# Performance work log

Hardware: AMD Instinct MI355X
Metric: run time of the kernel (lower is better)

The kernel has to match this reference:

```python
import jax, jax.numpy as jnp
import numpy as np


def setup_inputs() -> dict:
    key = jax.random.key(0)
    ks = jax.random.split(key, 9)
    B, T, C, H = 4, 2048, 1024, 16
    hd = C // H  # 64
    s = 0.02
    return {
        "x": jax.random.normal(ks[0], (B, T, C), dtype=jnp.float32),
        "Wq": jax.random.normal(ks[1], (H, C, hd), dtype=jnp.float32) * s,
        "bq": jax.random.normal(ks[2], (H, hd), dtype=jnp.float32) * s,
        "Wk": jax.random.normal(ks[3], (H, C, hd), dtype=jnp.float32) * s,
        "bk": jax.random.normal(ks[4], (H, hd), dtype=jnp.float32) * s,
        "Wv": jax.random.normal(ks[5], (H, C, hd), dtype=jnp.float32) * s,
        "bv": jax.random.normal(ks[6], (H, hd), dtype=jnp.float32) * s,
        "Wp": jax.random.normal(ks[7], (C, C), dtype=jnp.float32) * s,
        "bp": jax.random.normal(ks[8], (C,), dtype=jnp.float32) * s,
    }


def reference(x, Wq, bq, Wk, bk, Wv, bv, Wp, bp):
    B, T, C = x.shape
    # per-head projections, batched over heads: [B,H,T,hd]
    q = jnp.einsum('btc,hcd->bhtd', x, Wq) + bq[None, :, None, :]
    k = jnp.einsum('btc,hcd->bhtd', x, Wk) + bk[None, :, None, :]
    v = jnp.einsum('btc,hcd->bhtd', x, Wv) + bv[None, :, None, :]
    # NOTE: original scales by full embed dim C (not head_size) -- faithful quirk
    scale = jnp.asarray(C, x.dtype) ** -0.5
    wei = jnp.einsum('bhtd,bhsd->bhts', q, k) * scale  # [B,H,T,T]
    causal = jnp.tril(jnp.ones((T, T), dtype=bool))
    wei = jnp.where(causal, wei, jnp.asarray(-jnp.inf, wei.dtype))
    wei = jax.nn.softmax(wei, axis=-1)
    out = jnp.einsum('bhts,bhsd->bhtd', wei, v)  # [B,H,T,hd]
    # concat heads along feature dim -> [B,T,C]
    out = out.transpose(0, 2, 1, 3).reshape(B, T, C)
    return out @ Wp + bp
```

## Files before the change

kernel.cpp:

```cpp
#include <hip/hip_runtime.h>
#include <hip/hip_bf16.h>
#include <stdint.h>


typedef unsigned short u16;
typedef __attribute__((ext_vector_type(4))) float f32x4;
typedef __attribute__((ext_vector_type(8))) __bf16 bf16x8;
typedef __attribute__((ext_vector_type(2))) __bf16 bf16x2;

#define DEV static __device__ __forceinline__

DEV u16 f2bf(float f) {
  uint32_t u = __builtin_bit_cast(uint32_t, f);
  return (u16)((u + 0x7FFFu + ((u >> 16) & 1u)) >> 16);
}

DEV uint pack2(float a, float b) {
  bf16x2 v;
  v.x = (__bf16)a;
  v.y = (__bf16)b;
  return __builtin_bit_cast(uint, v);
}

#if __has_builtin(__builtin_amdgcn_exp2f)
DEV float fexp2(float x) { return __builtin_amdgcn_exp2f(x); }
#else
DEV float fexp2(float x) { return __expf(x * 0.69314718056f); }
#endif

DEV void gload_lds16(const void* g, void* lds) {
  auto gp = reinterpret_cast<const __attribute__((address_space(1))) uint32_t*>(
      reinterpret_cast<uintptr_t>(g));
  auto lp = reinterpret_cast<__attribute__((address_space(3))) uint32_t*>(
      static_cast<uint32_t>(reinterpret_cast<uintptr_t>(lds)));
  __builtin_amdgcn_global_load_lds(gp, lp, 16, 0, 0);
}

DEV f32x4 mfma16(bf16x8 a, bf16x8 b, f32x4 c) {
  return __builtin_amdgcn_mfma_f32_16x16x32_bf16(a, b, c, 0, 0, 0);
}

DEV void bar() {
  asm volatile("" ::: "memory");
  __builtin_amdgcn_s_barrier();
  asm volatile("" ::: "memory");
}

#define LD8(p) (*reinterpret_cast<const bf16x8*>(p))
#define LDU4(p) (*reinterpret_cast<const uint4*>(p))


__global__ void cvt_x_kernel(const float* __restrict__ x, u16* __restrict__ xb, int n8) {
  int i = blockIdx.x * blockDim.x + threadIdx.x;
  int stride = gridDim.x * blockDim.x;
  for (; i < n8; i += stride) {
    const float4* xp = reinterpret_cast<const float4*>(x) + 2 * (size_t)i;
    float4 a = xp[0], b = xp[1];
    uint4 o;
    o.x = pack2(a.x, a.y);
    o.y = pack2(a.z, a.w);
    o.z = pack2(b.x, b.y);
    o.w = pack2(b.z, b.w);
    reinterpret_cast<uint4*>(xb)[i] = o;
  }
}

__global__ void cvt_wqkv_kernel(const float* __restrict__ Wq, const float* __restrict__ Wk,
                                const float* __restrict__ Wv, const float* __restrict__ bq,
                                const float* __restrict__ bk, const float* __restrict__ bv,
                                u16* __restrict__ wt, float* __restrict__ biasq) {
  __shared__ u16 tle[64 * 72];
  const int tid = threadIdx.x;
  const int ct = blockIdx.x;
  const int h = blockIdx.y;
  const int which = blockIdx.z;
  const float* W = (which == 0) ? Wq : (which == 1) ? Wk : Wv;
  const float* Bb = (which == 0) ? bq : (which == 1) ? bk : bv;
  const float scl = (which == 0) ? 0.045084220027780106f : 1.0f;
#pragma unroll
  for (int i = 0; i < 4; ++i) {
    int idx = i * 256 + tid;
    int c_l = idx >> 4, d4 = (idx & 15) * 4;
    float4 v = *reinterpret_cast<const float4*>(&W[((size_t)(h * 1024 + ct * 64 + c_l)) * 64 + d4]);
    tle[(d4 + 0) * 72 + c_l] = f2bf(v.x * scl);
    tle[(d4 + 1) * 72 + c_l] = f2bf(v.y * scl);
    tle[(d4 + 2) * 72 + c_l] = f2bf(v.z * scl);
    tle[(d4 + 3) * 72 + c_l] = f2bf(v.w * scl);
  }
  __syncthreads();
#pragma unroll
  for (int i = 0; i < 2; ++i) {
    int idx = i * 256 + tid;
    int d_o = idx >> 3, c8 = (idx & 7) * 8;
    uint4 v = LDU4(&tle[d_o * 72 + c8]);
    *reinterpret_cast<uint4*>(&wt[(size_t)(which * 1024 + h * 64 + d_o) * 1024 + ct * 64 + c8]) = v;
  }
  if (ct == 0 && tid < 64) biasq[which * 1024 + h * 64 + tid] = Bb[h * 64 + tid] * scl;
}

__global__ void cvt_wp_kernel(const float* __restrict__ Wp, u16* __restrict__ wpt) {
  __shared__ u16 tle[64 * 72];
  const int tid = threadIdx.x;
  const int ct = blockIdx.x;
  const int nt = blockIdx.y;
#pragma unroll
  for (int i = 0; i < 4; ++i) {
    int idx = i * 256 + tid;
    int c_l = idx >> 4, n4 = (idx & 15) * 4;
    float4 v = *reinterpret_cast<const float4*>(&Wp[(size_t)(ct * 64 + c_l) * 1024 + nt * 64 + n4]);
    tle[(n4 + 0) * 72 + c_l] = f2bf(v.x);
    tle[(n4 + 1) * 72 + c_l] = f2bf(v.y);
    tle[(n4 + 2) * 72 + c_l] = f2bf(v.z);
    tle[(n4 + 3) * 72 + c_l] = f2bf(v.w);
  }
  __syncthreads();
#pragma unroll
  for (int i = 0; i < 2; ++i) {
    int idx = i * 256 + tid;
    int n_o = idx >> 3, c8 = (idx & 7) * 8;
    uint4 v = LDU4(&tle[n_o * 72 + c8]);
    *reinterpret_cast<uint4*>(&wpt[(size_t)(nt * 64 + n_o) * 1024 + ct * 64 + c8]) = v;
  }
}

__global__ __launch_bounds__(256)
void transpose_v_kernel(const u16* __restrict__ qkv, u16* __restrict__ vT) {
  __shared__ alignas(16) u16 tle[64 * 72];
  const int tid = threadIdx.x;
  const int tt = blockIdx.x;
  const int h = blockIdx.y;
  const int bb = blockIdx.z;
  const size_t rbase = ((size_t)bb * 2048 + tt * 64) * 3072 + 2048 + h * 64;
#pragma unroll
  for (int i = 0; i < 2; ++i) {
    int idx = i * 256 + tid;
    int s = idx >> 3, c8 = (idx & 7) * 8;
    *reinterpret_cast<uint4*>(&tle[s * 72 + c8]) = LDU4(&qkv[rbase + (size_t)s * 3072 + c8]);
  }
  __syncthreads();
#pragma unroll
  for (int i = 0; i < 2; ++i) {
    int idx = i * 256 + tid;
    int d = idx >> 3, cb = idx & 7;
    uint4 o;
    o.x = (uint)tle[(2 * cb + 0) * 72 + d] | ((uint)tle[(16 + 2 * cb + 0) * 72 + d] << 16);
    o.y = (uint)tle[(32 + 2 * cb + 0) * 72 + d] | ((uint)tle[(48 + 2 * cb + 0) * 72 + d] << 16);
    o.z = (uint)tle[(2 * cb + 1) * 72 + d] | ((uint)tle[(16 + 2 * cb + 1) * 72 + d] << 16);
    o.w = (uint)tle[(32 + 2 * cb + 1) * 72 + d] | ((uint)tle[(48 + 2 * cb + 1) * 72 + d] << 16);
    *reinterpret_cast<uint4*>(
        &vT[((size_t)(bb * 16 + h) * 64 + d) * 2048 + tt * 64 + cb * 8]) = o;
  }
}


template <bool OUT_F32>
__global__ __launch_bounds__(512, 2)
void gemm9_kernel(const u16* __restrict__ A, const u16* __restrict__ Bt,
                  const float* __restrict__ bias, void* __restrict__ Cout,
                  int M, int N, int K, int nbn) {
  __shared__ alignas(16) u16 LA[2 * 8192];
  __shared__ alignas(16) u16 LB[3 * 16384];

  const int tid = threadIdx.x;
  const int lane = tid & 63;
  const int wave = tid >> 6;
  const int wm = wave >> 2;
  const int wn = wave & 3;
  const int fr = lane & 15;
  const int kg = lane >> 4;
  const int f7 = fr & 7;
  const int r4 = kg * 4;

  const int nwg = gridDim.x;
  const int swz = (blockIdx.x & 7) * (nwg >> 3) + (blockIdx.x >> 3);
  const int m0 = (swz / nbn) * 128;
  const int n0 = (swz % nbn) * 256;

  const int NT = K >> 6;

  const int srow = tid >> 3;
  const int sgcol = ((tid & 7) ^ (srow & 7)) << 3;
  const size_t aOff = (size_t)(m0 + srow) * K + sgcol;
  const size_t bOff = (size_t)(n0 + srow) * K + sgcol;
  const int ldst = tid * 8;

  auto stageA = [&](int kt, u16* labuf) {
    gload_lds16(A + aOff + (size_t)kt * 64, labuf + ldst);
    gload_lds16(A + aOff + (size_t)64 * K + (size_t)kt * 64, labuf + 4096 + ldst);
  };
  auto stageB = [&](int kt, u16* lbbuf) {
    gload_lds16(Bt + bOff + (size_t)kt * 64, lbbuf + ldst);
    gload_lds16(Bt + bOff + (size_t)64 * K + (size_t)kt * 64, lbbuf + 4096 + ldst);
    gload_lds16(Bt + bOff + (size_t)128 * K + (size_t)kt * 64, lbbuf + 8192 + ldst);
    gload_lds16(Bt + bOff + (size_t)192 * K + (size_t)kt * 64, lbbuf + 12288 + ldst);
  };

  f32x4 acc[4][4] = {};

  stageA(0, LA);
  stageB(0, LB);
  if (NT > 1) {
    stageB(1, LB + 16384);
    asm volatile("s_waitcnt vmcnt(4)" ::: "memory");
  } else {
    asm volatile("s_waitcnt vmcnt(0)" ::: "memory");
  }
  bar();

  for (int kt = 0; kt < NT; ++kt) {
    const bool st1 = (kt + 1 < NT);
    const bool st2 = (kt + 2 < NT);
    u16* laCur = LA + (kt & 1) * 8192;
    u16* lbCur = LB + (kt % 3) * 16384;

    if (st1) stageA(kt + 1, LA + ((kt + 1) & 1) * 8192);
    if (st2) stageB(kt + 2, LB + ((kt + 2) % 3) * 16384);

    bf16x8 aF[4][2], bF[4][2];
#pragma unroll
    for (int m = 0; m < 4; ++m)
#pragma unroll
      for (int ks = 0; ks < 2; ++ks)
        aF[m][ks] = LD8(&laCur[wm * 4096 + (m * 16 + fr) * 64 + (((ks * 4 + kg) ^ f7) << 3)]);
#pragma unroll
    for (int n = 0; n < 4; ++n)
#pragma unroll
      for (int ks = 0; ks < 2; ++ks)
        bF[n][ks] = LD8(&lbCur[wn * 4096 + (n * 16 + fr) * 64 + (((ks * 4 + kg) ^ f7) << 3)]);

    __builtin_amdgcn_s_setprio(1);
#pragma unroll
    for (int ks = 0; ks < 2; ++ks)
#pragma unroll
      for (int m = 0; m < 4; ++m)
#pragma unroll
        for (int n = 0; n < 4; ++n)
          acc[m][n] = mfma16(aF[m][ks], bF[n][ks], acc[m][n]);
    __builtin_amdgcn_s_setprio(0);

    if (st1) {
      if (st2) asm volatile("s_waitcnt vmcnt(4)" ::: "memory");
      else     asm volatile("s_waitcnt vmcnt(0)" ::: "memory");
      bar();
    }
  }

#pragma unroll
  for (int m = 0; m < 4; ++m) {
    const int row = m0 + wm * 64 + m * 16 + r4;
#pragma unroll
    for (int n = 0; n < 4; ++n) {
      const int col = n0 + wn * 64 + n * 16 + fr;
      const float bv = bias[col];
#pragma unroll
      for (int r = 0; r < 4; ++r) {
        float v = acc[m][n][r] + bv;
        size_t off = (size_t)(row + r) * N + col;
        if constexpr (OUT_F32) reinterpret_cast<float*>(Cout)[off] = v;
        else                   reinterpret_cast<u16*>(Cout)[off] = f2bf(v);
      }
    }
  }
}


__global__ __launch_bounds__(128, 2)
void attn_kernel(const u16* __restrict__ qkv, const u16* __restrict__ vT,
                 u16* __restrict__ obuf) {
  __shared__ alignas(16) u16 Ks[64 * 72];
  __shared__ alignas(16) u16 Vs[64 * 72];
  __shared__ alignas(16) u16 Ps[2][32 * 72];

  const int tid = threadIdx.x;
  const int lane = tid & 63;
  const int wave = tid >> 6;

  const int gid = blockIdx.x;
  const int xcd = gid & 7;
  const int jj = gid >> 3;
  const int g = xcd * 8 + (jj >> 4);
  const int pair = jj & 15;
  const int bb = g >> 4;
  const int h = g & 15;

  const size_t baseQ = (size_t)bb * 2048 * 3072 + h * 64;
  const size_t baseK = baseQ + 1024;
  const size_t baseVt = (size_t)(bb * 16 + h) * 64 * 2048;

  const int fr = lane & 15;
  const int kg8 = (lane >> 4) * 8;
  const int qw32 = wave * 32;
  const int r4 = (lane >> 4) * 4;

  const int rrA = tid >> 3;
  const int cA8 = (tid & 7) * 8;
  const size_t gK = (size_t)rrA * 3072 + cA8;
  const size_t gV = (size_t)rrA * 2048 + cA8;
  const int lof = rrA * 72 + cA8;
  u16* __restrict__ Pw = &Ps[wave][0];

  for (int half = 0; half < 2; ++half) {
    const int qt = half ? (31 - pair) : pair;
    const int q0 = qt * 64;
    const int nt = qt + 1;

    const u16* qrow0 = &qkv[baseQ + (size_t)(q0 + qw32 + fr) * 3072 + kg8];
    bf16x8 aq00 = LD8(qrow0), aq01 = LD8(qrow0 + 32);
    const u16* qrow1 = qrow0 + 16 * 3072;
    bf16x8 aq10 = LD8(qrow1), aq11 = LD8(qrow1 + 32);

    float lsA0 = 0.f, lsA1 = 0.f, lsA2 = 0.f, lsA3 = 0.f;
    float lsB0 = 0.f, lsB1 = 0.f, lsB2 = 0.f, lsB3 = 0.f;
    f32x4 oA0 = {}, oA1 = {}, oA2 = {}, oA3 = {};
    f32x4 oB0 = {}, oB1 = {}, oB2 = {}, oB3 = {};

    uint4 kr0 = LDU4(&qkv[baseK + gK]);
    uint4 kr1 = LDU4(&qkv[baseK + gK + 49152]);
    uint4 kr2 = LDU4(&qkv[baseK + gK + 98304]);
    uint4 kr3 = LDU4(&qkv[baseK + gK + 147456]);
    uint4 vr0 = LDU4(&vT[baseVt + gV]);
    uint4 vr1 = LDU4(&vT[baseVt + gV + 32768]);
    uint4 vr2 = LDU4(&vT[baseVt + gV + 65536]);
    uint4 vr3 = LDU4(&vT[baseVt + gV + 98304]);

    for (int t = 0; t < nt; ++t) {
      __syncthreads();
      *reinterpret_cast<uint4*>(&Ks[lof]) = kr0;
      *reinterpret_cast<uint4*>(&Ks[lof + 1152]) = kr1;
      *reinterpret_cast<uint4*>(&Ks[lof + 2304]) = kr2;
      *reinterpret_cast<uint4*>(&Ks[lof + 3456]) = kr3;
      *reinterpret_cast<uint4*>(&Vs[lof]) = vr0;
      *reinterpret_cast<uint4*>(&Vs[lof + 1152]) = vr1;
      *reinterpret_cast<uint4*>(&Vs[lof + 2304]) = vr2;
      *reinterpret_cast<uint4*>(&Vs[lof + 3456]) = vr3;
      if (t + 1 < nt) {
        const u16* nk = &qkv[baseK + (size_t)(t + 1) * 196608];
        const u16* nv = &vT[baseVt + (size_t)(t + 1) * 64];
        kr0 = LDU4(nk + gK);
        kr1 = LDU4(nk + gK + 49152);
        kr2 = LDU4(nk + gK + 98304);
        kr3 = LDU4(nk + gK + 147456);
        vr0 = LDU4(nv + gV);
        vr1 = LDU4(nv + gV + 32768);
        vr2 = LDU4(nv + gV + 65536);
        vr3 = LDU4(nv + gV + 98304);
      }
      __syncthreads();

      f32x4 sA0 = {}, sA1 = {}, sA2 = {}, sA3 = {};
      f32x4 sB0 = {}, sB1 = {}, sB2 = {}, sB3 = {};
      {
        bf16x8 b;
        __builtin_amdgcn_s_setprio(1);
        b = LD8(&Ks[(fr) * 72 + kg8]);           sA0 = mfma16(aq00, b, sA0); sB0 = mfma16(aq10, b, sB0);
        b = LD8(&Ks[(16 + fr) * 72 + kg8]);      sA1 = mfma16(aq00, b, sA1); sB1 = mfma16(aq10, b, sB1);
        b = LD8(&Ks[(32 + fr) * 72 + kg8]);      sA2 = mfma16(aq00, b, sA2); sB2 = mfma16(aq10, b, sB2);
        b = LD8(&Ks[(48 + fr) * 72 + kg8]);      sA3 = mfma16(aq00, b, sA3); sB3 = mfma16(aq10, b, sB3);
        b = LD8(&Ks[(fr) * 72 + 32 + kg8]);      sA0 = mfma16(aq01, b, sA0); sB0 = mfma16(aq11, b, sB0);
        b = LD8(&Ks[(16 + fr) * 72 + 32 + kg8]); sA1 = mfma16(aq01, b, sA1); sB1 = mfma16(aq11, b, sB1);
        b = LD8(&Ks[(32 + fr) * 72 + 32 + kg8]); sA2 = mfma16(aq01, b, sA2); sB2 = mfma16(aq11, b, sB2);
        b = LD8(&Ks[(48 + fr) * 72 + 32 + kg8]); sA3 = mfma16(aq01, b, sA3); sB3 = mfma16(aq11, b, sB3);
        __builtin_amdgcn_s_setprio(0);
      }

      const bool diag = (t == nt - 1);
#define SM_ROW_G(S0, S1, S2, S3, LS, RB, r)                                    \
      {                                                                        \
        const int qg = qw32 + RB + r4 + r;                                     \
        float p0 = fexp2(S0[r]);                                               \
        float p1 = fexp2(S1[r]);                                               \
        float p2 = fexp2(S2[r]);                                               \
        float p3 = fexp2(S3[r]);                                               \
        if (diag) {                                                            \
          if (fr > qg) p0 = 0.f;                                               \
          if (fr + 16 > qg) p1 = 0.f;                                          \
          if (fr + 32 > qg) p2 = 0.f;                                          \
          if (fr + 48 > qg) p3 = 0.f;                                          \
        }                                                                      \
        LS += (p0 + p1) + (p2 + p3);                                           \
        uint2 w;                                                               \
        w.x = pack2(p0, p1);                                                   \
        w.y = pack2(p2, p3);                                                   \
        *reinterpret_cast<uint2*>(&Pw[(RB + r4 + r) * 72 + fr * 4]) = w;       \
      }
      SM_ROW_G(sA0, sA1, sA2, sA3, lsA0, 0, 0)
      SM_ROW_G(sA0, sA1, sA2, sA3, lsA1, 0, 1)
      SM_ROW_G(sA0, sA1, sA2, sA3, lsA2, 0, 2)
      SM_ROW_G(sA0, sA1, sA2, sA3, lsA3, 0, 3)
      SM_ROW_G(sB0, sB1, sB2, sB3, lsB0, 16, 0)
      SM_ROW_G(sB0, sB1, sB2, sB3, lsB1, 16, 1)
      SM_ROW_G(sB0, sB1, sB2, sB3, lsB2, 16, 2)
      SM_ROW_G(sB0, sB1, sB2, sB3, lsB3, 16, 3)
#undef SM_ROW_G

      {
        bf16x8 pfA = LD8(&Pw[fr * 72 + kg8]);
        bf16x8 pfB = LD8(&Pw[(16 + fr) * 72 + kg8]);
        bf16x8 v;
        __builtin_amdgcn_s_setprio(1);
        v = LD8(&Vs[(fr) * 72 + kg8]);           oA0 = mfma16(pfA, v, oA0); oB0 = mfma16(pfB, v, oB0);
        v = LD8(&Vs[(16 + fr) * 72 + kg8]);      oA1 = mfma16(pfA, v, oA1); oB1 = mfma16(pfB, v, oB1);
        v = LD8(&Vs[(32 + fr) * 72 + kg8]);      oA2 = mfma16(pfA, v, oA2); oB2 = mfma16(pfB, v, oB2);
        v = LD8(&Vs[(48 + fr) * 72 + kg8]);      oA3 = mfma16(pfA, v, oA3); oB3 = mfma16(pfB, v, oB3);
        pfA = LD8(&Pw[fr * 72 + 32 + kg8]);
        pfB = LD8(&Pw[(16 + fr) * 72 + 32 + kg8]);
        v = LD8(&Vs[(fr) * 72 + 32 + kg8]);      oA0 = mfma16(pfA, v, oA0); oB0 = mfma16(pfB, v, oB0);
        v = LD8(&Vs[(16 + fr) * 72 + 32 + kg8]); oA1 = mfma16(pfA, v, oA1); oB1 = mfma16(pfB, v, oB1);
        v = LD8(&Vs[(32 + fr) * 72 + 32 + kg8]); oA2 = mfma16(pfA, v, oA2); oB2 = mfma16(pfB, v, oB2);
        v = LD8(&Vs[(48 + fr) * 72 + 32 + kg8]); oA3 = mfma16(pfA, v, oA3); oB3 = mfma16(pfB, v, oB3);
        __builtin_amdgcn_s_setprio(0);
      }
    }

#define EPI_G(O0, O1, O2, O3, LS, RB, r)                                       \
    {                                                                          \
      float s = LS;                                                            \
      s += __shfl_xor(s, 1);                                                   \
      s += __shfl_xor(s, 2);                                                   \
      s += __shfl_xor(s, 4);                                                   \
      s += __shfl_xor(s, 8);                                                   \
      const float inv = 1.0f / s;                                              \
      const int qg = q0 + qw32 + RB + r4 + r;                                  \
      const size_t rowoff = ((size_t)bb * 2048 + qg) * 1024 + h * 64;          \
      obuf[rowoff + fr] = f2bf(O0[r] * inv);                                   \
      obuf[rowoff + 16 + fr] = f2bf(O1[r] * inv);                              \
      obuf[rowoff + 32 + fr] = f2bf(O2[r] * inv);                              \
      obuf[rowoff + 48 + fr] = f2bf(O3[r] * inv);                              \
    }
    EPI_G(oA0, oA1, oA2, oA3, lsA0, 0, 0)
    EPI_G(oA0, oA1, oA2, oA3, lsA1, 0, 1)
    EPI_G(oA0, oA1, oA2, oA3, lsA2, 0, 2)
    EPI_G(oA0, oA1, oA2, oA3, lsA3, 0, 3)
    EPI_G(oB0, oB1, oB2, oB3, lsB0, 16, 0)
    EPI_G(oB0, oB1, oB2, oB3, lsB1, 16, 1)
    EPI_G(oB0, oB1, oB2, oB3, lsB2, 16, 2)
    EPI_G(oB0, oB1, oB2, oB3, lsB3, 16, 3)
#undef EPI_G
  }
}


extern "C" void kernel_launch(void* const* d_in, const int* in_sizes, int n_in,
                              void* d_out, int out_size, void* d_ws, size_t ws_size,
                              hipStream_t stream) {
  const float* x  = (const float*)d_in[0];
  const float* Wq = (const float*)d_in[1];
  const float* bq = (const float*)d_in[2];
  const float* Wk = (const float*)d_in[3];
  const float* bk = (const float*)d_in[4];
  const float* Wv = (const float*)d_in[5];
  const float* bv = (const float*)d_in[6];
  const float* Wp = (const float*)d_in[7];
  const float* bp = (const float*)d_in[8];

  char* ws = (char*)d_ws;
  size_t off = 0;
  auto alloc = [&](size_t bytes) -> void* {
    void* p = ws + off;
    off += (bytes + 255) & ~(size_t)255;
    return p;
  };
  u16*   xb     = (u16*)  alloc((size_t)8192 * 1024 * 2);
  u16*   wqkv_t = (u16*)  alloc((size_t)3072 * 1024 * 2);
  float* biasq  = (float*)alloc((size_t)3072 * 4);
  u16*   wpt    = (u16*)  alloc((size_t)1024 * 1024 * 2);
  u16*   qkv    = (u16*)  alloc((size_t)8192 * 3072 * 2);
  u16*   obuf   = (u16*)  alloc((size_t)8192 * 1024 * 2);
  u16*   vT     = xb;
  (void)ws_size; (void)in_sizes; (void)n_in; (void)out_size;

  cvt_x_kernel<<<2048, 256, 0, stream>>>(x, xb, 8192 * 1024 / 8);
  cvt_wqkv_kernel<<<dim3(16, 16, 3), 256, 0, stream>>>(Wq, Wk, Wv, bq, bk, bv, wqkv_t, biasq);
  cvt_wp_kernel<<<dim3(16, 16), 256, 0, stream>>>(Wp, wpt);
  gemm9_kernel<false><<<768, 512, 0, stream>>>(xb, wqkv_t, biasq, qkv, 8192, 3072, 1024, 12);
  transpose_v_kernel<<<dim3(32, 16, 4), 256, 0, stream>>>(qkv, vT);
  attn_kernel<<<1024, 128, 0, stream>>>(qkv, vT, obuf);
  gemm9_kernel<true><<<256, 512, 0, stream>>>(obuf, wpt, bp, d_out, 8192, 1024, 1024, 4);
}
```

Before: 156.6 us.

## Enlarge GEMM tile to 256x256 with double-buffered LDS pipeline

The GEMM block tile grows from 128x256 to 256x256, so each wave computes an 8x4 grid of MFMA tiles and reuses each loaded B fragment across twice as many A rows. The staging pipeline changes from triple-buffered B with one-ahead A to a plain double buffer for both operands, waiting on all loads before each barrier. Grid sizes are halved. This aims to cut global and LDS traffic per flop, but doubles accumulator registers and LDS use, which may lower occupancy. The shallower prefetch and the halved grids (128 blocks for the output projection) may also leave more load latency exposed and under-fill the CUs.

```diff
diff --git a/kernel.cpp b/kernel.cpp
--- a/kernel.cpp
+++ b/kernel.cpp
@@ -155,11 +155,11 @@
 
 template <bool OUT_F32>
 __global__ __launch_bounds__(512, 2)
-void gemm9_kernel(const u16* __restrict__ A, const u16* __restrict__ Bt,
-                  const float* __restrict__ bias, void* __restrict__ Cout,
-                  int M, int N, int K, int nbn) {
-  __shared__ alignas(16) u16 LA[2 * 8192];
-  __shared__ alignas(16) u16 LB[3 * 16384];
+void gemm11_kernel(const u16* __restrict__ A, const u16* __restrict__ Bt,
+                   const float* __restrict__ bias, void* __restrict__ Cout,
+                   int M, int N, int K, int nbn) {
+  __shared__ alignas(16) u16 LA[2 * 16384];
+  __shared__ alignas(16) u16 LB[2 * 16384];
 
   const int tid = threadIdx.x;
   const int lane = tid & 63;
@@ -173,7 +173,7 @@
 
   const int nwg = gridDim.x;
   const int swz = (blockIdx.x & 7) * (nwg >> 3) + (blockIdx.x >> 3);
-  const int m0 = (swz / nbn) * 128;
+  const int m0 = (swz / nbn) * 256;
   const int n0 = (swz % nbn) * 256;
 
   const int NT = K >> 6;
@@ -184,70 +184,63 @@
   const size_t bOff = (size_t)(n0 + srow) * K + sgcol;
   const int ldst = tid * 8;
 
-  auto stageA = [&](int kt, u16* labuf) {
-    gload_lds16(A + aOff + (size_t)kt * 64, labuf + ldst);
-    gload_lds16(A + aOff + (size_t)64 * K + (size_t)kt * 64, labuf + 4096 + ldst);
+  auto stageA = [&](int kt, u16* d) {
+    gload_lds16(A + aOff + (size_t)kt * 64, d + ldst);
+    gload_lds16(A + aOff + (size_t)64 * K + (size_t)kt * 64, d + 4096 + ldst);
+    gload_lds16(A + aOff + (size_t)128 * K + (size_t)kt * 64, d + 8192 + ldst);
+    gload_lds16(A + aOff + (size_t)192 * K + (size_t)kt * 64, d + 12288 + ldst);
   };
-  auto stageB = [&](int kt, u16* lbbuf) {
-    gload_lds16(Bt + bOff + (size_t)kt * 64, lbbuf + ldst);
-    gload_lds16(Bt + bOff + (size_t)64 * K + (size_t)kt * 64, lbbuf + 4096 + ldst);
-    gload_lds16(Bt + bOff + (size_t)128 * K + (size_t)kt * 64, lbbuf + 8192 + ldst);
-    gload_lds16(Bt + bOff + (size_t)192 * K + (size_t)kt * 64, lbbuf + 12288 + ldst);
+  auto stageB = [&](int kt, u16* d) {
+    gload_lds16(Bt + bOff + (size_t)kt * 64, d + ldst);
+    gload_lds16(Bt + bOff + (size_t)64 * K + (size_t)kt * 64, d + 4096 + ldst);
+    gload_lds16(Bt + bOff + (size_t)128 * K + (size_t)kt * 64, d + 8192 + ldst);
+    gload_lds16(Bt + bOff + (size_t)192 * K + (size_t)kt * 64, d + 12288 + ldst);
   };
 
-  f32x4 acc[4][4] = {};
+  f32x4 acc[8][4] = {};
 
   stageA(0, LA);
   stageB(0, LB);
-  if (NT > 1) {
-    stageB(1, LB + 16384);
-    asm volatile("s_waitcnt vmcnt(4)" ::: "memory");
-  } else {
-    asm volatile("s_waitcnt vmcnt(0)" ::: "memory");
-  }
+  asm volatile("s_waitcnt vmcnt(0)" ::: "memory");
   bar();
 
   for (int kt = 0; kt < NT; ++kt) {
     const bool st1 = (kt + 1 < NT);
-    const bool st2 = (kt + 2 < NT);
-    u16* laCur = LA + (kt & 1) * 8192;
-    u16* lbCur = LB + (kt % 3) * 16384;
-
-    if (st1) stageA(kt + 1, LA + ((kt + 1) & 1) * 8192);
-    if (st2) stageB(kt + 2, LB + ((kt + 2) % 3) * 16384);
-
-    bf16x8 aF[4][2], bF[4][2];
-#pragma unroll
-    for (int m = 0; m < 4; ++m)
-#pragma unroll
-      for (int ks = 0; ks < 2; ++ks)
-        aF[m][ks] = LD8(&laCur[wm * 4096 + (m * 16 + fr) * 64 + (((ks * 4 + kg) ^ f7) << 3)]);
-#pragma unroll
-    for (int n = 0; n < 4; ++n)
-#pragma unroll
-      for (int ks = 0; ks < 2; ++ks)
-        bF[n][ks] = LD8(&lbCur[wn * 4096 + (n * 16 + fr) * 64 + (((ks * 4 + kg) ^ f7) << 3)]);
-
-    __builtin_amdgcn_s_setprio(1);
-#pragma unroll
-    for (int ks = 0; ks < 2; ++ks)
-#pragma unroll
-      for (int m = 0; m < 4; ++m)
+    u16* la = LA + (kt & 1) * 16384;
+    u16* lb = LB + (kt & 1) * 16384;
+
+    if (st1) {
+      stageA(kt + 1, LA + ((kt + 1) & 1) * 16384);
+      stageB(kt + 1, LB + ((kt + 1) & 1) * 16384);
+    }
+
+#pragma unroll
+    for (int ks = 0; ks < 2; ++ks) {
+      const int ko = ((ks * 4 + kg) ^ f7) << 3;
+      bf16x8 bfr[4];
+#pragma unroll
+      for (int n = 0; n < 4; ++n)
+        bfr[n] = LD8(&lb[(wn * 64 + n * 16 + fr) * 64 + ko]);
+      __builtin_amdgcn_s_setprio(1);
+#pragma unroll
+      for (int m = 0; m < 8; ++m) {
+        bf16x8 a = LD8(&la[(wm * 128 + m * 16 + fr) * 64 + ko]);
 #pragma unroll
         for (int n = 0; n < 4; ++n)
-          acc[m][n] = mfma16(aF[m][ks], bF[n][ks], acc[m][n]);
-    __builtin_amdgcn_s_setprio(0);
+          acc[m][n] = mfma16(a, bfr[n], acc[m][n]);
+      }
+      __builtin_amdgcn_s_setprio(0);
+    }
 
     if (st1) {
-      if (st2) asm volatile("s_waitcnt vmcnt(4)" ::: "memory");
-      else     asm volatile("s_waitcnt vmcnt(0)" ::: "memory");
+      asm volatile("s_waitcnt vmcnt(0)" ::: "memory");
       bar();
     }
   }
 
 #pragma unroll
-  for (int m = 0; m < 4; ++m) {
-    const int row = m0 + wm * 64 + m * 16 + r4;
+  for (int m = 0; m < 8; ++m) {
+    const int row = m0 + wm * 128 + m * 16 + r4;
 #pragma unroll
     for (int n = 0; n < 4; ++n) {
       const int col = n0 + wn * 64 + n * 16 + fr;
@@ -472,8 +465,8 @@
   cvt_x_kernel<<<2048, 256, 0, stream>>>(x, xb, 8192 * 1024 / 8);
   cvt_wqkv_kernel<<<dim3(16, 16, 3), 256, 0, stream>>>(Wq, Wk, Wv, bq, bk, bv, wqkv_t, biasq);
   cvt_wp_kernel<<<dim3(16, 16), 256, 0, stream>>>(Wp, wpt);
-  gemm9_kernel<false><<<768, 512, 0, stream>>>(xb, wqkv_t, biasq, qkv, 8192, 3072, 1024, 12);
+  gemm11_kernel<false><<<384, 512, 0, stream>>>(xb, wqkv_t, biasq, qkv, 8192, 3072, 1024, 12);
   transpose_v_kernel<<<dim3(32, 16, 4), 256, 0, stream>>>(qkv, vT);
   attn_kernel<<<1024, 128, 0, stream>>>(qkv, vT, obuf);
-  gemm9_kernel<true><<<256, 512, 0, stream>>>(obuf, wpt, bp, d_out, 8192, 1024, 1024, 4);
-}
+  gemm11_kernel<true><<<128, 512, 0, stream>>>(obuf, wpt, bp, d_out, 8192, 1024, 1024, 4);
+}
```

New measurement: 171.8 us. +9.7%, slower.

## Add 256x256-tile GEMM kernel with split-phase prefetch for QKV projection

Applied to the files above, without the earlier changes.

Adds a new GEMM kernel with 256x256 output tiles, in which each wave computes 128x64 via 8x4 MFMA accumulators. It double-buffers A and B in LDS and interleaves the next tile's global-to-LDS loads across four MFMA phases using setprio. The QKV projection now uses it with 384 workgroups instead of 768, which raises data reuse per LDS load and cuts global traffic. The cost is doubled accumulator registers (128 floats per lane), more LDS (128KB per block, which may limit occupancy to one block), and fewer workgroups than the 256 CUs can absorb evenly, leaving 384 blocks spread over 256 CUs.

```diff
diff --git a/kernel.cpp b/kernel.cpp
--- a/kernel.cpp
+++ b/kernel.cpp
@@ -155,11 +155,11 @@
 
 template <bool OUT_F32>
 __global__ __launch_bounds__(512, 2)
-void gemm9_kernel(const u16* __restrict__ A, const u16* __restrict__ Bt,
-                  const float* __restrict__ bias, void* __restrict__ Cout,
-                  int M, int N, int K, int nbn) {
-  __shared__ alignas(16) u16 LA[2 * 8192];
-  __shared__ alignas(16) u16 LB[3 * 16384];
+void gemm12_kernel(const u16* __restrict__ A, const u16* __restrict__ Bt,
+                   const float* __restrict__ bias, void* __restrict__ Cout,
+                   int M, int N, int K, int nbn) {
+  __shared__ alignas(16) u16 LA[2 * 16384];
+  __shared__ alignas(16) u16 LB[2 * 16384];
 
   const int tid = threadIdx.x;
   const int lane = tid & 63;
@@ -173,9 +173,144 @@
 
   const int nwg = gridDim.x;
   const int swz = (blockIdx.x & 7) * (nwg >> 3) + (blockIdx.x >> 3);
+  const int m0 = (swz / nbn) * 256;
+  const int n0 = (swz % nbn) * 256;
+  const int NT = K >> 6;
+
+  const int srow = tid >> 3;
+  const int sgcol = ((tid & 7) ^ (srow & 7)) << 3;
+  const size_t aOff = (size_t)(m0 + srow) * K + sgcol;
+  const size_t bOff = (size_t)(n0 + srow) * K + sgcol;
+  const int ldst = tid * 8;
+
+  auto stA = [&](int kt, int q, u16* d) {
+    gload_lds16(A + aOff + (size_t)(q * 64) * K + (size_t)kt * 64, d + q * 4096 + ldst);
+  };
+  auto stB = [&](int kt, int q, u16* d) {
+    gload_lds16(Bt + bOff + (size_t)(q * 64) * K + (size_t)kt * 64, d + q * 4096 + ldst);
+  };
+
+  f32x4 acc[8][4] = {};
+
+  stA(0, 0, LA); stA(0, 1, LA); stA(0, 2, LA); stA(0, 3, LA);
+  stB(0, 0, LB); stB(0, 1, LB); stB(0, 2, LB); stB(0, 3, LB);
+  if (NT > 1) {
+    stA(1, 0, LA + 16384); stA(1, 2, LA + 16384);
+    asm volatile("s_waitcnt vmcnt(2)" ::: "memory");
+  } else {
+    asm volatile("s_waitcnt vmcnt(0)" ::: "memory");
+  }
+  bar();
+
+  for (int kt = 0; kt < NT; ++kt) {
+    u16* la = LA + (kt & 1) * 16384;
+    u16* lb = LB + (kt & 1) * 16384;
+    u16* laN = LA + ((kt + 1) & 1) * 16384;
+    u16* lbN = LB + ((kt + 1) & 1) * 16384;
+    const int ko0 = (kg ^ f7) << 3;
+    const int ko1 = ((4 + kg) ^ f7) << 3;
+    const bool st1 = (kt + 1 < NT);
+    const bool st2 = (kt + 2 < NT);
+    bf16x8 afr[4], bfr[4];
+
+#pragma unroll
+    for (int m = 0; m < 4; ++m) afr[m] = LD8(&la[(wm * 128 + m * 16 + fr) * 64 + ko0]);
+#pragma unroll
+    for (int n = 0; n < 4; ++n) bfr[n] = LD8(&lb[(wn * 64 + n * 16 + fr) * 64 + ko0]);
+    if (st1) { stA(kt + 1, 1, laN); stA(kt + 1, 3, laN); }
+    bar();
+    __builtin_amdgcn_s_setprio(1);
+#pragma unroll
+    for (int m = 0; m < 4; ++m)
+#pragma unroll
+      for (int n = 0; n < 4; ++n) acc[m][n] = mfma16(afr[m], bfr[n], acc[m][n]);
+    __builtin_amdgcn_s_setprio(0);
+    bar();
+
+#pragma unroll
+    for (int m = 0; m < 4; ++m) afr[m] = LD8(&la[(wm * 128 + (m + 4) * 16 + fr) * 64 + ko0]);
+    if (st1) { stB(kt + 1, 0, lbN); stB(kt + 1, 1, lbN); }
+    bar();
+    __builtin_amdgcn_s_setprio(1);
+#pragma unroll
+    for (int m = 0; m < 4; ++m)
+#pragma unroll
+      for (int n = 0; n < 4; ++n) acc[m + 4][n] = mfma16(afr[m], bfr[n], acc[m + 4][n]);
+    __builtin_amdgcn_s_setprio(0);
+    bar();
+
+#pragma unroll
+    for (int m = 0; m < 4; ++m) afr[m] = LD8(&la[(wm * 128 + m * 16 + fr) * 64 + ko1]);
+#pragma unroll
+    for (int n = 0; n < 4; ++n) bfr[n] = LD8(&lb[(wn * 64 + n * 16 + fr) * 64 + ko1]);
+    if (st1) { stB(kt + 1, 2, lbN); stB(kt + 1, 3, lbN); }
+    bar();
+    __builtin_amdgcn_s_setprio(1);
+#pragma unroll
+    for (int m = 0; m < 4; ++m)
+#pragma unroll
+      for (int n = 0; n < 4; ++n) acc[m][n] = mfma16(afr[m], bfr[n], acc[m][n]);
+    __builtin_amdgcn_s_setprio(0);
+    bar();
+
+#pragma unroll
+    for (int m = 0; m < 4; ++m) afr[m] = LD8(&la[(wm * 128 + (m + 4) * 16 + fr) * 64 + ko1]);
+    if (st2) { stA(kt + 2, 0, la); stA(kt + 2, 2, la); }
+    if (st1) {
+      if (st2) asm volatile("s_waitcnt vmcnt(2)" ::: "memory");
+      else     asm volatile("s_waitcnt vmcnt(0)" ::: "memory");
+    }
+    bar();
+    __builtin_amdgcn_s_setprio(1);
+#pragma unroll
+    for (int m = 0; m < 4; ++m)
+#pragma unroll
+      for (int n = 0; n < 4; ++n) acc[m + 4][n] = mfma16(afr[m], bfr[n], acc[m + 4][n]);
+    __builtin_amdgcn_s_setprio(0);
+    bar();
+  }
+
+#pragma unroll
+  for (int m = 0; m < 8; ++m) {
+    const int row = m0 + wm * 128 + m * 16 + r4;
+#pragma unroll
+    for (int n = 0; n < 4; ++n) {
+      const int col = n0 + wn * 64 + n * 16 + fr;
+      const float bv = bias[col];
+#pragma unroll
+      for (int r = 0; r < 4; ++r) {
+        float v = acc[m][n][r] + bv;
+        size_t off = (size_t)(row + r) * N + col;
+        if constexpr (OUT_F32) reinterpret_cast<float*>(Cout)[off] = v;
+        else                   reinterpret_cast<u16*>(Cout)[off] = f2bf(v);
+      }
+    }
+  }
+}
+
+
+template <bool OUT_F32>
+__global__ __launch_bounds__(512, 2)
+void gemm9_kernel(const u16* __restrict__ A, const u16* __restrict__ Bt,
+                  const float* __restrict__ bias, void* __restrict__ Cout,
+                  int M, int N, int K, int nbn) {
+  __shared__ alignas(16) u16 LA[2 * 8192];
+  __shared__ alignas(16) u16 LB[3 * 16384];
+
+  const int tid = threadIdx.x;
+  const int lane = tid & 63;
+  const int wave = tid >> 6;
+  const int wm = wave >> 2;
+  const int wn = wave & 3;
+  const int fr = lane & 15;
+  const int kg = lane >> 4;
+  const int f7 = fr & 7;
+  const int r4 = kg * 4;
+
+  const int nwg = gridDim.x;
+  const int swz = (blockIdx.x & 7) * (nwg >> 3) + (blockIdx.x >> 3);
   const int m0 = (swz / nbn) * 128;
   const int n0 = (swz % nbn) * 256;
-
   const int NT = K >> 6;
 
   const int srow = tid >> 3;
@@ -472,7 +607,7 @@
   cvt_x_kernel<<<2048, 256, 0, stream>>>(x, xb, 8192 * 1024 / 8);
   cvt_wqkv_kernel<<<dim3(16, 16, 3), 256, 0, stream>>>(Wq, Wk, Wv, bq, bk, bv, wqkv_t, biasq);
   cvt_wp_kernel<<<dim3(16, 16), 256, 0, stream>>>(Wp, wpt);
-  gemm9_kernel<false><<<768, 512, 0, stream>>>(xb, wqkv_t, biasq, qkv, 8192, 3072, 1024, 12);
+  gemm12_kernel<false><<<384, 512, 0, stream>>>(xb, wqkv_t, biasq, qkv, 8192, 3072, 1024, 12);
   transpose_v_kernel<<<dim3(32, 16, 4), 256, 0, stream>>>(qkv, vT);
   attn_kernel<<<1024, 128, 0, stream>>>(qkv, vT, obuf);
   gemm9_kernel<true><<<256, 512, 0, stream>>>(obuf, wpt, bp, d_out, 8192, 1024, 1024, 4);
```

Result: slower. 163.9 us (+4.7%).

## Add smaller-LDS double-buffered GEMM with K=32 tiles for QKV projection

Applied to the files above, without the earlier changes.

Adds a new GEMM kernel for the QKV projection that uses 32-wide K tiles with double buffering instead of 64-wide tiles with a larger triple-buffered B stage. The LDS footprint drops so launch bounds can request four blocks per CU, trading per-iteration work for more resident waves to hide latency. It also uses a new XOR swizzle suited to the 32-element row width. The risk is twice as many barriers and vmcnt waits per K loop, with less MFMA work between them.

```diff
diff --git a/kernel.cpp b/kernel.cpp
--- a/kernel.cpp
+++ b/kernel.cpp
@@ -154,6 +154,105 @@
 
 
 template <bool OUT_F32>
+__global__ __launch_bounds__(512, 4)
+void gemm13_kernel(const u16* __restrict__ A, const u16* __restrict__ Bt,
+                   const float* __restrict__ bias, void* __restrict__ Cout,
+                   int M, int N, int K, int nbn) {
+  __shared__ alignas(16) u16 LA[2 * 4096];
+  __shared__ alignas(16) u16 LB[2 * 8192];
+
+  const int tid = threadIdx.x;
+  const int lane = tid & 63;
+  const int wave = tid >> 6;
+  const int wm = wave >> 2;
+  const int wn = wave & 3;
+  const int fr = lane & 15;
+  const int kg = lane >> 4;
+  const int r4 = kg * 4;
+
+  const int nwg = gridDim.x;
+  const int swz = (blockIdx.x & 7) * (nwg >> 3) + (blockIdx.x >> 3);
+  const int m0 = (swz / nbn) * 128;
+  const int n0 = (swz % nbn) * 256;
+  const int NT = K >> 5;
+
+  const int srow = tid >> 2;
+  const int sgcol = (((tid & 3) ^ ((srow >> 1) & 3)) << 3);
+  const size_t aOff = (size_t)(m0 + srow) * K + sgcol;
+  const size_t bOff = (size_t)(n0 + srow) * K + sgcol;
+  const int ldst = tid * 8;
+
+  auto stageA = [&](int kt, u16* d) {
+    gload_lds16(A + aOff + (size_t)kt * 32, d + ldst);
+  };
+  auto stageB = [&](int kt, u16* d) {
+    gload_lds16(Bt + bOff + (size_t)kt * 32, d + ldst);
+    gload_lds16(Bt + bOff + (size_t)128 * K + (size_t)kt * 32, d + 4096 + ldst);
+  };
+
+  f32x4 acc[4][4] = {};
+
+  stageA(0, LA);
+  stageB(0, LB);
+  asm volatile("s_waitcnt vmcnt(0)" ::: "memory");
+  bar();
+
+  for (int kt = 0; kt < NT; ++kt) {
+    const bool st1 = (kt + 1 < NT);
+    u16* la = LA + (kt & 1) * 4096;
+    u16* lb = LB + (kt & 1) * 8192;
+
+    if (st1) {
+      stageA(kt + 1, LA + ((kt + 1) & 1) * 4096);
+      stageB(kt + 1, LB + ((kt + 1) & 1) * 8192);
+    }
+
+    bf16x8 aF[4], bF[4];
+#pragma unroll
+    for (int m = 0; m < 4; ++m) {
+      const int R = wm * 64 + m * 16 + fr;
+      aF[m] = LD8(&la[R * 32 + ((kg ^ ((R >> 1) & 3)) << 3)]);
+    }
+#pragma unroll
+    for (int n = 0; n < 4; ++n) {
+      const int R = wn * 64 + n * 16 + fr;
+      bF[n] = LD8(&lb[R * 32 + ((kg ^ ((R >> 1) & 3)) << 3)]);
+    }
+
+    __builtin_amdgcn_s_setprio(1);
+#pragma unroll
+    for (int m = 0; m < 4; ++m)
+#pragma unroll
+      for (int n = 0; n < 4; ++n)
+        acc[m][n] = mfma16(aF[m], bF[n], acc[m][n]);
+    __builtin_amdgcn_s_setprio(0);
+
+    if (st1) {
+      asm volatile("s_waitcnt vmcnt(0)" ::: "memory");
+      bar();
+    }
+  }
+
+#pragma unroll
+  for (int m = 0; m < 4; ++m) {
+    const int row = m0 + wm * 64 + m * 16 + r4;
+#pragma unroll
+    for (int n = 0; n < 4; ++n) {
+      const int col = n0 + wn * 64 + n * 16 + fr;
+      const float bv = bias[col];
+#pragma unroll
+      for (int r = 0; r < 4; ++r) {
+        float v = acc[m][n][r] + bv;
+        size_t off = (size_t)(row + r) * N + col;
+        if constexpr (OUT_F32) reinterpret_cast<float*>(Cout)[off] = v;
+        else                   reinterpret_cast<u16*>(Cout)[off] = f2bf(v);
+      }
+    }
+  }
+}
+
+
+template <bool OUT_F32>
 __global__ __launch_bounds__(512, 2)
 void gemm9_kernel(const u16* __restrict__ A, const u16* __restrict__ Bt,
                   const float* __restrict__ bias, void* __restrict__ Cout,
@@ -175,7 +274,6 @@
   const int swz = (blockIdx.x & 7) * (nwg >> 3) + (blockIdx.x >> 3);
   const int m0 = (swz / nbn) * 128;
   const int n0 = (swz % nbn) * 256;
-
   const int NT = K >> 6;
 
   const int srow = tid >> 3;
@@ -472,7 +570,7 @@
   cvt_x_kernel<<<2048, 256, 0, stream>>>(x, xb, 8192 * 1024 / 8);
   cvt_wqkv_kernel<<<dim3(16, 16, 3), 256, 0, stream>>>(Wq, Wk, Wv, bq, bk, bv, wqkv_t, biasq);
   cvt_wp_kernel<<<dim3(16, 16), 256, 0, stream>>>(Wp, wpt);
-  gemm9_kernel<false><<<768, 512, 0, stream>>>(xb, wqkv_t, biasq, qkv, 8192, 3072, 1024, 12);
+  gemm13_kernel<false><<<768, 512, 0, stream>>>(xb, wqkv_t, biasq, qkv, 8192, 3072, 1024, 12);
   transpose_v_kernel<<<dim3(32, 16, 4), 256, 0, stream>>>(qkv, vT);
   attn_kernel<<<1024, 128, 0, stream>>>(qkv, vT, obuf);
   gemm9_kernel<true><<<256, 512, 0, stream>>>(obuf, wpt, bp, d_out, 8192, 1024, 1024, 4);
```

Result: no change. 158.1 us (+1.0%).
